# Optimization experiments

Hardware: AMD Instinct MI355X
Metric: run time of the kernel (lower is better)

## Reference

```python
import jax, jax.numpy as jnp
import numpy as np

NUM_REGIONS = 64
K_NEIGHBORS = 5
REGION_LAMBDA = 0.02
SPATIAL_LAMBDA = 0.0005


def setup_inputs() -> dict:
    key = jax.random.key(0)
    k1, k2, k3 = jax.random.split(key, 3)
    B = 16384
    c_points = jax.random.normal(k1, (B, 3), dtype=jnp.float32)
    coords_std = jax.random.normal(k2, (B, 3), dtype=jnp.float32)
    region_ids = jax.random.randint(k3, (B,), 0, NUM_REGIONS, dtype=jnp.int32)
    return {"c_points": c_points, "coords_std": coords_std, "region_ids": region_ids}


def _region_loss(c_points, region_ids):
    # Equivalent to per-region pairwise dispersion via segment reductions:
    # 2 * sum||c - mean_r||^2 / (max(n_r*(n_r-1)/2, 1) * xdim), summed over regions.
    dtype = c_points.dtype
    xdim = jnp.asarray(c_points.shape[1], dtype)
    ones = jnp.ones(c_points.shape[0], dtype)
    counts = jax.ops.segment_sum(ones, region_ids, num_segments=NUM_REGIONS)          # [R]
    sums = jax.ops.segment_sum(c_points, region_ids, num_segments=NUM_REGIONS)        # [R,3]
    sqs = jax.ops.segment_sum(c_points * c_points, region_ids, num_segments=NUM_REGIONS)  # [R,3]
    safe_n = jnp.maximum(counts, 1.0)
    mean = sums / safe_n[:, None]
    sum_sq_centered = jnp.sum(sqs - counts[:, None] * mean * mean, axis=1)             # [R]
    n_pairs = counts * (counts - 1.0) * 0.5
    denom = jnp.maximum(n_pairs, 1.0) * xdim
    per_region = jnp.where(counts > 1.0, 2.0 * sum_sq_centered / denom, 0.0)
    return jnp.asarray(REGION_LAMBDA, dtype) * jnp.sum(per_region)


def _spatial_loss(c_points, coords_std):
    # Dense pairwise squared distances, exclude self, KNN gather, mean squared diff of cuts.
    dtype = c_points.dtype
    B = coords_std.shape[0]
    xdim = jnp.asarray(c_points.shape[1], dtype)
    c2 = jnp.sum(coords_std * coords_std, axis=1, keepdims=True)                       # [B,1]
    d2 = c2 - 2.0 * (coords_std @ coords_std.T) + c2.T                                 # [B,B]
    big = jnp.max(d2) + 1.0
    diag = jnp.arange(B)
    d2 = d2.at[diag, diag].set(big)
    _, idxs = jax.lax.top_k(-d2, K_NEIGHBORS)                                          # [B,k]
    c_nb = c_points[idxs]                                                              # [B,k,3]
    diffs = c_points[:, None, :] - c_nb
    sq = jnp.sum(diffs * diffs, axis=2)                                                # [B,k]
    loss = jnp.mean(jnp.mean(sq, axis=1))
    return jnp.asarray(SPATIAL_LAMBDA, dtype) * (loss / jnp.maximum(xdim, 1.0))


def reference(c_points, coords_std, region_ids):
    return _region_loss(c_points, region_ids) + _spatial_loss(c_points, coords_std)
```

## Files before the change

kernel.cpp:

```cpp
#include <hip/hip_runtime.h>
#include <stdint.h>

#define B_N    16384
#define NREG   64
#define KNB    5
#define SAMPLE 4096
#define NSUB   16
#define SUBLEN (SAMPLE / NSUB)
#define NCH    32
#define CHLEN  (B_N / NCH)
#define MRGBLK 256
#define SENT   0xFFFF

static __device__ __forceinline__ float inf32() { return __int_as_float(0x7f800000); }
static __device__ __forceinline__ float med3(float a, float b, float c) {
    return __builtin_amdgcn_fmed3f(a, b, c);
}

#define MINS5(nv)                      \
    {                                  \
        s4 = med3(s3, s4, (nv));       \
        s3 = med3(s2, s3, (nv));       \
        s2 = med3(s1, s2, (nv));       \
        s1 = med3(s0, s1, (nv));       \
        s0 = fminf(s0, (nv));          \
    }

#define INS5(nv, jj)                                                        \
    {                                                                       \
        bool c4 = (nv) < s4, c3 = (nv) < s3, c2 = (nv) < s2,                \
             c1 = (nv) < s1, c0 = (nv) < s0;                                \
        s4 = c3 ? s3 : (c4 ? (nv) : s4);  i4 = c3 ? i3 : (c4 ? (jj) : i4);  \
        s3 = c2 ? s2 : (c3 ? (nv) : s3);  i3 = c2 ? i2 : (c3 ? (jj) : i3);  \
        s2 = c1 ? s1 : (c2 ? (nv) : s2);  i2 = c1 ? i1 : (c2 ? (jj) : i2);  \
        s1 = c0 ? s0 : (c1 ? (nv) : s1);  i1 = c0 ? i0 : (c1 ? (jj) : i1);  \
        s0 = c0 ? (nv) : s0;              i0 = c0 ? (jj) : i0;              \
    }

__global__ __launch_bounds__(256) void scan_region_kernel(const float* __restrict__ c,
                                                          const float* __restrict__ x,
                                                          const int* __restrict__ ids,
                                                          float4* __restrict__ pre,
                                                          float* __restrict__ tauv,
                                                          float* __restrict__ wsreg,
                                                          int* __restrict__ counter) {
    const int blk = blockIdx.x;
    const int tid = threadIdx.x;

    if (blk >= 1024) {
        const int r = blk - 1024;
        if (r == 0 && tid == 0) *counter = 0;
        {
            int j = r * 256 + tid;
            float jx = x[3 * j + 0], jy = x[3 * j + 1], jz = x[3 * j + 2];
            pre[j] = make_float4(-2.f * jx, -2.f * jy, -2.f * jz,
                                 jx * jx + jy * jy + jz * jz);
        }
        float cnt = 0.f, sx = 0.f, sy = 0.f, sz = 0.f, sxx = 0.f, syy = 0.f, szz = 0.f;
        for (int i = tid; i < B_N; i += 256) {
            int id = ids[i];
            float m = (id == r) ? 1.0f : 0.0f;
            float px = c[3 * i + 0], py = c[3 * i + 1], pz = c[3 * i + 2];
            cnt += m;
            sx += m * px;  sy += m * py;  sz += m * pz;
            sxx += m * px * px;  syy += m * py * py;  szz += m * pz * pz;
        }
        for (int off = 32; off > 0; off >>= 1) {
            cnt += __shfl_down(cnt, off);
            sx  += __shfl_down(sx, off);
            sy  += __shfl_down(sy, off);
            sz  += __shfl_down(sz, off);
            sxx += __shfl_down(sxx, off);
            syy += __shfl_down(syy, off);
            szz += __shfl_down(szz, off);
        }
        __shared__ float sb[4][7];
        const int lane = tid & 63, w = tid >> 6;
        if (lane == 0) {
            sb[w][0] = cnt; sb[w][1] = sx; sb[w][2] = sy; sb[w][3] = sz;
            sb[w][4] = sxx; sb[w][5] = syy; sb[w][6] = szz;
        }
        __syncthreads();
        if (tid == 0) {
            float C = 0, SX = 0, SY = 0, SZ = 0, SXX = 0, SYY = 0, SZZ = 0;
            for (int i = 0; i < 4; i++) {
                C += sb[i][0]; SX += sb[i][1]; SY += sb[i][2]; SZ += sb[i][3];
                SXX += sb[i][4]; SYY += sb[i][5]; SZZ += sb[i][6];
            }
            float safe = fmaxf(C, 1.0f);
            float mx = SX / safe, my = SY / safe, mz = SZ / safe;
            float ssc = (SXX - C * mx * mx) + (SYY - C * my * my) + (SZZ - C * mz * mz);
            float npairs = C * (C - 1.0f) * 0.5f;
            float denom = fmaxf(npairs, 1.0f) * 3.0f;
            wsreg[r] = (C > 1.0f) ? (2.0f * ssc / denom) : 0.0f;
        }
        return;
    }

    __shared__ float4 tile[SUBLEN];
    const int qb = blk & 63;
    const int sub = blk >> 6;
    const int q = qb * 256 + tid;
    const int j0 = sub * SUBLEN;
    {
        int j = j0 + tid;
        float jx = x[3 * j + 0], jy = x[3 * j + 1], jz = x[3 * j + 2];
        tile[tid] = make_float4(-2.f * jx, -2.f * jy, -2.f * jz,
                                jx * jx + jy * jy + jz * jz);
    }
    const float qx = x[3 * q + 0], qy = x[3 * q + 1], qz = x[3 * q + 2];
    __syncthreads();

    float s0 = inf32(), s1 = inf32(), s2 = inf32(), s3 = inf32(), s4 = inf32();

    for (int jb = 0; jb < SUBLEN; jb += 8) {
        float dt[8];
#pragma unroll
        for (int u = 0; u < 8; ++u) {
            float4 pj = tile[jb + u];
            dt[u] = fmaf(pj.x, qx, fmaf(pj.y, qy, fmaf(pj.z, qz, pj.w)));
        }
#pragma unroll
        for (int u = 0; u < 8; ++u) {
            float nv = ((j0 + jb + u) != q) ? dt[u] : inf32();
            MINS5(nv);
        }
    }
    tauv[(sub * 5 + 0) * B_N + q] = s0;
    tauv[(sub * 5 + 1) * B_N + q] = s1;
    tauv[(sub * 5 + 2) * B_N + q] = s2;
    tauv[(sub * 5 + 3) * B_N + q] = s3;
    tauv[(sub * 5 + 4) * B_N + q] = s4;
}

__global__ __launch_bounds__(256) void tau_merge_kernel(const float* __restrict__ tauv,
                                                        float* __restrict__ tau) {
    const int q = blockIdx.x * 256 + threadIdx.x;
    float s0 = inf32(), s1 = inf32(), s2 = inf32(), s3 = inf32(), s4 = inf32();
#pragma unroll 8
    for (int n = 0; n < NSUB * 5; ++n) {
        float v = tauv[n * B_N + q];
        MINS5(v);
    }
    int b = __float_as_int(s4);
    b += (b >= 0) ? 1 : -1;
    tau[q] = __int_as_float(b);
}

__global__ __launch_bounds__(256) void spatial_kernel(const float4* __restrict__ pre,
                                                      const float* __restrict__ tau,
                                                      unsigned short* __restrict__ cand) {
    __shared__ float4 tile[CHLEN];
    const int tid = threadIdx.x;
    const int qb = blockIdx.x & 63;
    const int ch = blockIdx.x >> 6;
    const int q = qb * 256 + tid;
    const int jbase = ch * CHLEN;

#pragma unroll
    for (int i = 0; i < CHLEN / 256; ++i)
        tile[tid + i * 256] = pre[jbase + tid + i * 256];

    const float4 pq = pre[q];
    const float qx = -0.5f * pq.x, qy = -0.5f * pq.y, qz = -0.5f * pq.z;
    const float t = tau[q];
    __syncthreads();

    float s0 = t, s1 = t, s2 = t, s3 = t, s4 = t;
    int i0 = SENT, i1 = SENT, i2 = SENT, i3 = SENT, i4 = SENT;

    for (int jb = 0; jb < CHLEN; jb += 8) {
        float dt[8];
#pragma unroll
        for (int u = 0; u < 8; ++u) {
            float4 pj = tile[jb + u];
            dt[u] = fmaf(pj.x, qx, fmaf(pj.y, qy, fmaf(pj.z, qz, pj.w)));
        }
        float m = fminf(fminf(fminf(dt[0], dt[1]), fminf(dt[2], dt[3])),
                        fminf(fminf(dt[4], dt[5]), fminf(dt[6], dt[7])));
        if (__builtin_expect(__any(m < s4), 0)) {
#pragma unroll
            for (int u = 0; u < 8; ++u) {
                if (__any(dt[u] < s4)) {
                    int j = jbase + jb + u;
                    bool p = (dt[u] < s4) && (j != q);
                    float nv = p ? dt[u] : inf32();
                    INS5(nv, j);
                }
            }
        }
    }
    cand[(ch * 5 + 0) * B_N + q] = (unsigned short)i0;
    cand[(ch * 5 + 1) * B_N + q] = (unsigned short)i1;
    cand[(ch * 5 + 2) * B_N + q] = (unsigned short)i2;
    cand[(ch * 5 + 3) * B_N + q] = (unsigned short)i3;
    cand[(ch * 5 + 4) * B_N + q] = (unsigned short)i4;
}

__global__ __launch_bounds__(256) void merge_kernel(const float* __restrict__ c,
                                                    const float4* __restrict__ pre,
                                                    const unsigned short* __restrict__ cand,
                                                    const float* __restrict__ wsreg,
                                                    float* __restrict__ spart,
                                                    int* __restrict__ counter,
                                                    float* __restrict__ out) {
    const int tid = threadIdx.x;
    const int blk = blockIdx.x;
    const int qloc = tid >> 2;
    const int part = tid & 3;
    const int q = blk * 64 + qloc;
    const float4 pq = pre[q];
    const float qx = -0.5f * pq.x, qy = -0.5f * pq.y, qz = -0.5f * pq.z;

    __shared__ float dm[64][4][5];
    __shared__ unsigned short im[64][4][5];

    {
        float s0 = inf32(), s1 = inf32(), s2 = inf32(), s3 = inf32(), s4 = inf32();
        int i0 = SENT & 0x3FFF, i1 = i0, i2 = i0, i3 = i0, i4 = i0;
        const int n0 = part * (NCH / 4) * 5;
#pragma unroll 8
        for (int n = n0; n < n0 + (NCH / 4) * 5; ++n) {
            int cd = (int)cand[n * B_N + q];
            int safe = cd & 0x3FFF;
            float4 pj = pre[safe];
            float d = fmaf(pj.x, qx, fmaf(pj.y, qy, fmaf(pj.z, qz, pj.w)));
            float nv = (cd != SENT) ? d : inf32();
            INS5(nv, safe);
        }
        dm[qloc][part][0] = s0; im[qloc][part][0] = (unsigned short)i0;
        dm[qloc][part][1] = s1; im[qloc][part][1] = (unsigned short)i1;
        dm[qloc][part][2] = s2; im[qloc][part][2] = (unsigned short)i2;
        dm[qloc][part][3] = s3; im[qloc][part][3] = (unsigned short)i3;
        dm[qloc][part][4] = s4; im[qloc][part][4] = (unsigned short)i4;
    }
    __syncthreads();

    float acc = 0.f;
    if (part == 0) {
        float s0 = inf32(), s1 = inf32(), s2 = inf32(), s3 = inf32(), s4 = inf32();
        int i0 = 0, i1 = 0, i2 = 0, i3 = 0, i4 = 0;
#pragma unroll
        for (int p = 0; p < 4; ++p)
#pragma unroll
            for (int k = 0; k < 5; ++k) {
                float nv = dm[qloc][p][k];
                int jj = (int)im[qloc][p][k];
                INS5(nv, jj);
            }
        const float cx = c[3 * q + 0], cy = c[3 * q + 1], cz = c[3 * q + 2];
        int ks[5] = {i0, i1, i2, i3, i4};
#pragma unroll
        for (int n = 0; n < KNB; ++n) {
            int nb = ks[n];
            float dx = cx - c[3 * nb + 0];
            float dy = cy - c[3 * nb + 1];
            float dz = cz - c[3 * nb + 2];
            acc += dx * dx + dy * dy + dz * dz;
        }
    }
    acc += __shfl_down(acc, 32);
    acc += __shfl_down(acc, 16);
    acc += __shfl_down(acc, 8);
    acc += __shfl_down(acc, 4);
    __shared__ float wsum[4];
    __shared__ int last;
    const int lane = tid & 63, w = tid >> 6;
    if (lane == 0) wsum[w] = acc;
    __syncthreads();
    if (tid == 0) {
        float bs = wsum[0] + wsum[1] + wsum[2] + wsum[3];
        atomicExch(&spart[blk], bs);
        __threadfence();
        int old = atomicAdd(counter, 1);
        last = (old == MRGBLK - 1);
    }
    __syncthreads();
    if (last) {
        float s = atomicAdd(&spart[tid], 0.0f);
        float r = (tid < NREG) ? wsreg[tid] : 0.f;
        for (int off = 32; off > 0; off >>= 1) {
            s += __shfl_down(s, off);
            r += __shfl_down(r, off);
        }
        __shared__ float fb[4];
        if (lane == 0) fb[w] = s;
        __syncthreads();
        if (tid == 0) {
            float S = fb[0] + fb[1] + fb[2] + fb[3];
            float spatial_mean = S / (float)(B_N * KNB);
            out[0] = 0.02f * r + 0.0005f * (spatial_mean / 3.0f);
        }
    }
}

extern "C" void kernel_launch(void* const* d_in, const int* in_sizes, int n_in,
                              void* d_out, int out_size, void* d_ws, size_t ws_size,
                              hipStream_t stream) {
    const float* c  = (const float*)d_in[0];
    const float* x  = (const float*)d_in[1];
    const int* ids  = (const int*)d_in[2];
    float* out = (float*)d_out;

    char* ws = (char*)d_ws;
    float4* pre = (float4*)ws;
    float* tauv = (float*)(ws + (size_t)B_N * 16);
    unsigned short* cand =
        (unsigned short*)((char*)tauv + (size_t)NSUB * 5 * B_N * 4);
    float* tau = (float*)((char*)cand + (size_t)NCH * 5 * B_N * 2);
    float* wsreg = tau + B_N;
    float* spart = wsreg + NREG;
    int* counter = (int*)(spart + MRGBLK);

    hipLaunchKernelGGL(scan_region_kernel, dim3(1088), dim3(256), 0, stream,
                       c, x, ids, pre, tauv, wsreg, counter);
    hipLaunchKernelGGL(tau_merge_kernel, dim3(64), dim3(256), 0, stream, tauv, tau);
    hipLaunchKernelGGL(spatial_kernel, dim3(64 * NCH), dim3(256), 0, stream, pre, tau, cand);
    hipLaunchKernelGGL(merge_kernel, dim3(MRGBLK), dim3(256), 0, stream, c, pre, cand,
                       wsreg, spart, counter, out);
}
```

Before: 92.45 us.

## Fuse tau merge, spatial scan and candidate merge into one kernel

The tau threshold merge is folded into the spatial kernel, so every block recomputes the per-query threshold from tauv instead of reading it from a separate kernel's output. The final candidate merge now runs in the last-arriving block of each query group, found through per-group atomic counters, and a global counter picks the block that does the final reduction. This removes two kernel launches and their inter-kernel gaps. In exchange, tauv reads are repeated 32 times over, and the final merge runs with one thread per query in only 64 blocks, which serializes the tail.

Result: slower. 139.6 us (+51.0%).

```diff
diff --git a/kernel.cpp b/kernel.cpp
--- a/kernel.cpp
+++ b/kernel.cpp
@@ -9,7 +9,6 @@
 #define SUBLEN (SAMPLE / NSUB)
 #define NCH    32
 #define CHLEN  (B_N / NCH)
-#define MRGBLK 256
 #define SENT   0xFFFF
 
 static __device__ __forceinline__ float inf32() { return __int_as_float(0x7f800000); }
@@ -43,13 +42,17 @@
                                                           float4* __restrict__ pre,
                                                           float* __restrict__ tauv,
                                                           float* __restrict__ wsreg,
+                                                          int* __restrict__ qbcount,
                                                           int* __restrict__ counter) {
     const int blk = blockIdx.x;
     const int tid = threadIdx.x;
 
     if (blk >= 1024) {
         const int r = blk - 1024;
-        if (r == 0 && tid == 0) *counter = 0;
+        if (tid == 0) {
+            qbcount[r] = 0;
+            if (r == 0) *counter = 0;
+        }
         {
             int j = r * 256 + tid;
             float jx = x[3 * j + 0], jy = x[3 * j + 1], jz = x[3 * j + 2];
@@ -133,23 +136,15 @@
     tauv[(sub * 5 + 4) * B_N + q] = s4;
 }
 
-__global__ __launch_bounds__(256) void tau_merge_kernel(const float* __restrict__ tauv,
-                                                        float* __restrict__ tau) {
-    const int q = blockIdx.x * 256 + threadIdx.x;
-    float s0 = inf32(), s1 = inf32(), s2 = inf32(), s3 = inf32(), s4 = inf32();
-#pragma unroll 8
-    for (int n = 0; n < NSUB * 5; ++n) {
-        float v = tauv[n * B_N + q];
-        MINS5(v);
-    }
-    int b = __float_as_int(s4);
-    b += (b >= 0) ? 1 : -1;
-    tau[q] = __int_as_float(b);
-}
-
-__global__ __launch_bounds__(256) void spatial_kernel(const float4* __restrict__ pre,
-                                                      const float* __restrict__ tau,
-                                                      unsigned short* __restrict__ cand) {
+__global__ __launch_bounds__(256) void spatial_merge_kernel(const float* __restrict__ c,
+                                                            const float4* __restrict__ pre,
+                                                            const float* __restrict__ tauv,
+                                                            unsigned short* __restrict__ cand,
+                                                            const float* __restrict__ wsreg,
+                                                            float* __restrict__ spart,
+                                                            int* __restrict__ qbcount,
+                                                            int* __restrict__ counter,
+                                                            float* __restrict__ out) {
     __shared__ float4 tile[CHLEN];
     const int tid = threadIdx.x;
     const int qb = blockIdx.x & 63;
@@ -163,64 +158,72 @@
 
     const float4 pq = pre[q];
     const float qx = -0.5f * pq.x, qy = -0.5f * pq.y, qz = -0.5f * pq.z;
-    const float t = tau[q];
-    __syncthreads();
-
-    float s0 = t, s1 = t, s2 = t, s3 = t, s4 = t;
-    int i0 = SENT, i1 = SENT, i2 = SENT, i3 = SENT, i4 = SENT;
-
-    for (int jb = 0; jb < CHLEN; jb += 8) {
-        float dt[8];
-#pragma unroll
-        for (int u = 0; u < 8; ++u) {
-            float4 pj = tile[jb + u];
-            dt[u] = fmaf(pj.x, qx, fmaf(pj.y, qy, fmaf(pj.z, qz, pj.w)));
-        }
-        float m = fminf(fminf(fminf(dt[0], dt[1]), fminf(dt[2], dt[3])),
-                        fminf(fminf(dt[4], dt[5]), fminf(dt[6], dt[7])));
-        if (__builtin_expect(__any(m < s4), 0)) {
+
+    float t;
+    {
+        float s0 = inf32(), s1 = inf32(), s2 = inf32(), s3 = inf32(), s4 = inf32();
+#pragma unroll 8
+        for (int n = 0; n < NSUB * 5; ++n) {
+            float v = tauv[n * B_N + q];
+            MINS5(v);
+        }
+        int b = __float_as_int(s4);
+        b += (b >= 0) ? 1 : -1;
+        t = __int_as_float(b);
+    }
+    __syncthreads();
+
+    {
+        float s0 = t, s1 = t, s2 = t, s3 = t, s4 = t;
+        int i0 = SENT, i1 = SENT, i2 = SENT, i3 = SENT, i4 = SENT;
+
+        for (int jb = 0; jb < CHLEN; jb += 8) {
+            float dt[8];
 #pragma unroll
             for (int u = 0; u < 8; ++u) {
-                if (__any(dt[u] < s4)) {
-                    int j = jbase + jb + u;
-                    bool p = (dt[u] < s4) && (j != q);
-                    float nv = p ? dt[u] : inf32();
-                    INS5(nv, j);
+                float4 pj = tile[jb + u];
+                dt[u] = fmaf(pj.x, qx, fmaf(pj.y, qy, fmaf(pj.z, qz, pj.w)));
+            }
+            float m = fminf(fminf(fminf(dt[0], dt[1]), fminf(dt[2], dt[3])),
+                            fminf(fminf(dt[4], dt[5]), fminf(dt[6], dt[7])));
+            if (__builtin_expect(__any(m < s4), 0)) {
+#pragma unroll
+                for (int u = 0; u < 8; ++u) {
+                    if (__any(dt[u] < s4)) {
+                        int j = jbase + jb + u;
+                        bool p = (dt[u] < s4) && (j != q);
+                        float nv = p ? dt[u] : inf32();
+                        INS5(nv, j);
+                    }
                 }
             }
         }
-    }
-    cand[(ch * 5 + 0) * B_N + q] = (unsigned short)i0;
-    cand[(ch * 5 + 1) * B_N + q] = (unsigned short)i1;
-    cand[(ch * 5 + 2) * B_N + q] = (unsigned short)i2;
-    cand[(ch * 5 + 3) * B_N + q] = (unsigned short)i3;
-    cand[(ch * 5 + 4) * B_N + q] = (unsigned short)i4;
-}
-
-__global__ __launch_bounds__(256) void merge_kernel(const float* __restrict__ c,
-                                                    const float4* __restrict__ pre,
-                                                    const unsigned short* __restrict__ cand,
-                                                    const float* __restrict__ wsreg,
-                                                    float* __restrict__ spart,
-                                                    int* __restrict__ counter,
-                                                    float* __restrict__ out) {
-    const int tid = threadIdx.x;
-    const int blk = blockIdx.x;
-    const int qloc = tid >> 2;
-    const int part = tid & 3;
-    const int q = blk * 64 + qloc;
-    const float4 pq = pre[q];
-    const float qx = -0.5f * pq.x, qy = -0.5f * pq.y, qz = -0.5f * pq.z;
-
-    __shared__ float dm[64][4][5];
-    __shared__ unsigned short im[64][4][5];
-
+        cand[(ch * 5 + 0) * B_N + q] = (unsigned short)i0;
+        cand[(ch * 5 + 1) * B_N + q] = (unsigned short)i1;
+        cand[(ch * 5 + 2) * B_N + q] = (unsigned short)i2;
+        cand[(ch * 5 + 3) * B_N + q] = (unsigned short)i3;
+        cand[(ch * 5 + 4) * B_N + q] = (unsigned short)i4;
+    }
+
+    __shared__ int lastqb;
+    __syncthreads();
+    if (tid == 0) {
+        __threadfence();
+        int old = atomicAdd(&qbcount[qb], 1);
+        lastqb = (old == NCH - 1);
+    }
+    __syncthreads();
+    if (!lastqb) return;
+
+    if (tid == 0) __threadfence();
+    __syncthreads();
+
+    float acc = 0.f;
     {
         float s0 = inf32(), s1 = inf32(), s2 = inf32(), s3 = inf32(), s4 = inf32();
-        int i0 = SENT & 0x3FFF, i1 = i0, i2 = i0, i3 = i0, i4 = i0;
-        const int n0 = part * (NCH / 4) * 5;
+        int i0 = 0, i1 = 0, i2 = 0, i3 = 0, i4 = 0;
 #pragma unroll 8
-        for (int n = n0; n < n0 + (NCH / 4) * 5; ++n) {
+        for (int n = 0; n < NCH * 5; ++n) {
             int cd = (int)cand[n * B_N + q];
             int safe = cd & 0x3FFF;
             float4 pj = pre[safe];
@@ -228,26 +231,6 @@
             float nv = (cd != SENT) ? d : inf32();
             INS5(nv, safe);
         }
-        dm[qloc][part][0] = s0; im[qloc][part][0] = (unsigned short)i0;
-        dm[qloc][part][1] = s1; im[qloc][part][1] = (unsigned short)i1;
-        dm[qloc][part][2] = s2; im[qloc][part][2] = (unsigned short)i2;
-        dm[qloc][part][3] = s3; im[qloc][part][3] = (unsigned short)i3;
-        dm[qloc][part][4] = s4; im[qloc][part][4] = (unsigned short)i4;
-    }
-    __syncthreads();
-
-    float acc = 0.f;
-    if (part == 0) {
-        float s0 = inf32(), s1 = inf32(), s2 = inf32(), s3 = inf32(), s4 = inf32();
-        int i0 = 0, i1 = 0, i2 = 0, i3 = 0, i4 = 0;
-#pragma unroll
-        for (int p = 0; p < 4; ++p)
-#pragma unroll
-            for (int k = 0; k < 5; ++k) {
-                float nv = dm[qloc][p][k];
-                int jj = (int)im[qloc][p][k];
-                INS5(nv, jj);
-            }
         const float cx = c[3 * q + 0], cy = c[3 * q + 1], cz = c[3 * q + 2];
         int ks[5] = {i0, i1, i2, i3, i4};
 #pragma unroll
@@ -259,37 +242,37 @@
             acc += dx * dx + dy * dy + dz * dz;
         }
     }
-    acc += __shfl_down(acc, 32);
-    acc += __shfl_down(acc, 16);
-    acc += __shfl_down(acc, 8);
-    acc += __shfl_down(acc, 4);
+    for (int off = 32; off > 0; off >>= 1) acc += __shfl_down(acc, off);
     __shared__ float wsum[4];
-    __shared__ int last;
+    __shared__ int lastall;
     const int lane = tid & 63, w = tid >> 6;
     if (lane == 0) wsum[w] = acc;
     __syncthreads();
     if (tid == 0) {
         float bs = wsum[0] + wsum[1] + wsum[2] + wsum[3];
-        atomicExch(&spart[blk], bs);
+        atomicExch(&spart[qb], bs);
         __threadfence();
         int old = atomicAdd(counter, 1);
-        last = (old == MRGBLK - 1);
-    }
-    __syncthreads();
-    if (last) {
-        float s = atomicAdd(&spart[tid], 0.0f);
+        lastall = (old == 63);
+    }
+    __syncthreads();
+    if (!lastall) return;
+
+    {
+        float s = (tid < 64) ? atomicAdd(&spart[tid], 0.0f) : 0.f;
         float r = (tid < NREG) ? wsreg[tid] : 0.f;
         for (int off = 32; off > 0; off >>= 1) {
             s += __shfl_down(s, off);
             r += __shfl_down(r, off);
         }
-        __shared__ float fb[4];
-        if (lane == 0) fb[w] = s;
+        __shared__ float fb[4][2];
+        if (lane == 0) { fb[w][0] = s; fb[w][1] = r; }
         __syncthreads();
         if (tid == 0) {
-            float S = fb[0] + fb[1] + fb[2] + fb[3];
+            float S = fb[0][0] + fb[1][0] + fb[2][0] + fb[3][0];
+            float R = fb[0][1] + fb[1][1] + fb[2][1] + fb[3][1];
             float spatial_mean = S / (float)(B_N * KNB);
-            out[0] = 0.02f * r + 0.0005f * (spatial_mean / 3.0f);
+            out[0] = 0.02f * R + 0.0005f * (spatial_mean / 3.0f);
         }
     }
 }
@@ -307,15 +290,13 @@
     float* tauv = (float*)(ws + (size_t)B_N * 16);
     unsigned short* cand =
         (unsigned short*)((char*)tauv + (size_t)NSUB * 5 * B_N * 4);
-    float* tau = (float*)((char*)cand + (size_t)NCH * 5 * B_N * 2);
-    float* wsreg = tau + B_N;
+    float* wsreg = (float*)((char*)cand + (size_t)NCH * 5 * B_N * 2);
     float* spart = wsreg + NREG;
-    int* counter = (int*)(spart + MRGBLK);
+    int* qbcount = (int*)(spart + 64);
+    int* counter = qbcount + 64;
 
     hipLaunchKernelGGL(scan_region_kernel, dim3(1088), dim3(256), 0, stream,
-                       c, x, ids, pre, tauv, wsreg, counter);
-    hipLaunchKernelGGL(tau_merge_kernel, dim3(64), dim3(256), 0, stream, tauv, tau);
-    hipLaunchKernelGGL(spatial_kernel, dim3(64 * NCH), dim3(256), 0, stream, pre, tau, cand);
-    hipLaunchKernelGGL(merge_kernel, dim3(MRGBLK), dim3(256), 0, stream, c, pre, cand,
-                       wsreg, spart, counter, out);
+                       c, x, ids, pre, tauv, wsreg, qbcount, counter);
+    hipLaunchKernelGGL(spatial_merge_kernel, dim3(64 * NCH), dim3(256), 0, stream,
+                       c, pre, tauv, cand, wsreg, spart, qbcount, counter, out);
 }
```

## Use packed FP32 FMA with paired SoA tiles for distance evaluation

Applied to the files above, without the earlier changes.

Reference points are stored in pairs (two x's, two y's, two z's, two norms) so that v_pk_fma_f32 computes two squared distances per instruction in both the sampling scan and the candidate spatial pass. The aim is to halve the FMA instruction count in these compute-bound loops. A second change drops the self-exclusion select in scan blocks whose tile cannot contain the query. Costs are an extra pre-pass writing the paired layout, inline asm, and more workspace.

New measurement: 103.4 us. +11.9%, slower.

```diff
diff --git a/kernel.cpp b/kernel.cpp
--- a/kernel.cpp
+++ b/kernel.cpp
@@ -12,9 +12,21 @@
 #define MRGBLK 256
 #define SENT   0xFFFF
 
+typedef __attribute__((ext_vector_type(2))) float f32x2;
+
 static __device__ __forceinline__ float inf32() { return __int_as_float(0x7f800000); }
 static __device__ __forceinline__ float med3(float a, float b, float c) {
     return __builtin_amdgcn_fmed3f(a, b, c);
+}
+static __device__ __forceinline__ f32x2 pk_fma(f32x2 a, f32x2 b, f32x2 c) {
+    f32x2 d;
+    asm("v_pk_fma_f32 %0, %1, %2, %3" : "=v"(d) : "v"(a), "v"(b), "v"(c));
+    return d;
+}
+static __device__ __forceinline__ f32x2 pdist(float4 A, float4 B,
+                                              f32x2 qx2, f32x2 qy2, f32x2 qz2) {
+    f32x2 X = {A.x, A.y}, Y = {A.z, A.w}, Z = {B.x, B.y}, W = {B.z, B.w};
+    return pk_fma(X, qx2, pk_fma(Y, qy2, pk_fma(Z, qz2, W)));
 }
 
 #define MINS5(nv)                      \
@@ -41,6 +53,8 @@
                                                           const float* __restrict__ x,
                                                           const int* __restrict__ ids,
                                                           float4* __restrict__ pre,
+                                                          float4* __restrict__ gA,
+                                                          float4* __restrict__ gB,
                                                           float* __restrict__ tauv,
                                                           float* __restrict__ wsreg,
                                                           int* __restrict__ counter) {
@@ -55,6 +69,14 @@
             float jx = x[3 * j + 0], jy = x[3 * j + 1], jz = x[3 * j + 2];
             pre[j] = make_float4(-2.f * jx, -2.f * jy, -2.f * jz,
                                  jx * jx + jy * jy + jz * jz);
+            if ((tid & 1) == 0) {
+                float kx = x[3 * j + 3], ky = x[3 * j + 4], kz = x[3 * j + 5];
+                int p = j >> 1;
+                gA[p] = make_float4(-2.f * jx, -2.f * kx, -2.f * jy, -2.f * ky);
+                gB[p] = make_float4(-2.f * jz, -2.f * kz,
+                                    jx * jx + jy * jy + jz * jz,
+                                    kx * kx + ky * ky + kz * kz);
+            }
         }
         float cnt = 0.f, sx = 0.f, sy = 0.f, sz = 0.f, sxx = 0.f, syy = 0.f, szz = 0.f;
         for (int i = tid; i < B_N; i += 256) {
@@ -97,33 +119,50 @@
         return;
     }
 
-    __shared__ float4 tile[SUBLEN];
+    __shared__ float4 tA[SUBLEN / 2], tB[SUBLEN / 2];
     const int qb = blk & 63;
     const int sub = blk >> 6;
     const int q = qb * 256 + tid;
     const int j0 = sub * SUBLEN;
-    {
+    if ((tid & 1) == 0) {
         int j = j0 + tid;
-        float jx = x[3 * j + 0], jy = x[3 * j + 1], jz = x[3 * j + 2];
-        tile[tid] = make_float4(-2.f * jx, -2.f * jy, -2.f * jz,
-                                jx * jx + jy * jy + jz * jz);
+        float ax = x[3 * j + 0], ay = x[3 * j + 1], az = x[3 * j + 2];
+        float bx = x[3 * j + 3], by = x[3 * j + 4], bz = x[3 * j + 5];
+        int p = tid >> 1;
+        tA[p] = make_float4(-2.f * ax, -2.f * bx, -2.f * ay, -2.f * by);
+        tB[p] = make_float4(-2.f * az, -2.f * bz,
+                            ax * ax + ay * ay + az * az,
+                            bx * bx + by * by + bz * bz);
     }
     const float qx = x[3 * q + 0], qy = x[3 * q + 1], qz = x[3 * q + 2];
+    const f32x2 qx2 = {qx, qx}, qy2 = {qy, qy}, qz2 = {qz, qz};
     __syncthreads();
 
     float s0 = inf32(), s1 = inf32(), s2 = inf32(), s3 = inf32(), s4 = inf32();
 
-    for (int jb = 0; jb < SUBLEN; jb += 8) {
-        float dt[8];
-#pragma unroll
-        for (int u = 0; u < 8; ++u) {
-            float4 pj = tile[jb + u];
-            dt[u] = fmaf(pj.x, qx, fmaf(pj.y, qy, fmaf(pj.z, qz, pj.w)));
-        }
-#pragma unroll
-        for (int u = 0; u < 8; ++u) {
-            float nv = ((j0 + jb + u) != q) ? dt[u] : inf32();
-            MINS5(nv);
+    if (sub != (qb & 15) || qb >= 16) {
+        for (int jb = 0; jb < SUBLEN; jb += 8) {
+            const int p0 = jb >> 1;
+            f32x2 d0 = pdist(tA[p0 + 0], tB[p0 + 0], qx2, qy2, qz2);
+            f32x2 d1 = pdist(tA[p0 + 1], tB[p0 + 1], qx2, qy2, qz2);
+            f32x2 d2 = pdist(tA[p0 + 2], tB[p0 + 2], qx2, qy2, qz2);
+            f32x2 d3 = pdist(tA[p0 + 3], tB[p0 + 3], qx2, qy2, qz2);
+            MINS5(d0.x); MINS5(d0.y); MINS5(d1.x); MINS5(d1.y);
+            MINS5(d2.x); MINS5(d2.y); MINS5(d3.x); MINS5(d3.y);
+        }
+    } else {
+        for (int jb = 0; jb < SUBLEN; jb += 8) {
+            const int p0 = jb >> 1;
+            f32x2 d0 = pdist(tA[p0 + 0], tB[p0 + 0], qx2, qy2, qz2);
+            f32x2 d1 = pdist(tA[p0 + 1], tB[p0 + 1], qx2, qy2, qz2);
+            f32x2 d2 = pdist(tA[p0 + 2], tB[p0 + 2], qx2, qy2, qz2);
+            f32x2 d3 = pdist(tA[p0 + 3], tB[p0 + 3], qx2, qy2, qz2);
+            float dv[8] = {d0.x, d0.y, d1.x, d1.y, d2.x, d2.y, d3.x, d3.y};
+#pragma unroll
+            for (int u = 0; u < 8; ++u) {
+                float nv = ((j0 + jb + u) != q) ? dv[u] : inf32();
+                MINS5(nv);
+            }
         }
     }
     tauv[(sub * 5 + 0) * B_N + q] = s0;
@@ -148,21 +187,23 @@
 }
 
 __global__ __launch_bounds__(256) void spatial_kernel(const float4* __restrict__ pre,
+                                                      const float4* __restrict__ gA,
+                                                      const float4* __restrict__ gB,
                                                       const float* __restrict__ tau,
                                                       unsigned short* __restrict__ cand) {
-    __shared__ float4 tile[CHLEN];
+    __shared__ float4 tA[CHLEN / 2], tB[CHLEN / 2];
     const int tid = threadIdx.x;
     const int qb = blockIdx.x & 63;
     const int ch = blockIdx.x >> 6;
     const int q = qb * 256 + tid;
     const int jbase = ch * CHLEN;
 
-#pragma unroll
-    for (int i = 0; i < CHLEN / 256; ++i)
-        tile[tid + i * 256] = pre[jbase + tid + i * 256];
+    tA[tid] = gA[(jbase >> 1) + tid];
+    tB[tid] = gB[(jbase >> 1) + tid];
 
     const float4 pq = pre[q];
     const float qx = -0.5f * pq.x, qy = -0.5f * pq.y, qz = -0.5f * pq.z;
+    const f32x2 qx2 = {qx, qx}, qy2 = {qy, qy}, qz2 = {qz, qz};
     const float t = tau[q];
     __syncthreads();
 
@@ -170,21 +211,21 @@
     int i0 = SENT, i1 = SENT, i2 = SENT, i3 = SENT, i4 = SENT;
 
     for (int jb = 0; jb < CHLEN; jb += 8) {
-        float dt[8];
-#pragma unroll
-        for (int u = 0; u < 8; ++u) {
-            float4 pj = tile[jb + u];
-            dt[u] = fmaf(pj.x, qx, fmaf(pj.y, qy, fmaf(pj.z, qz, pj.w)));
-        }
-        float m = fminf(fminf(fminf(dt[0], dt[1]), fminf(dt[2], dt[3])),
-                        fminf(fminf(dt[4], dt[5]), fminf(dt[6], dt[7])));
+        const int p0 = jb >> 1;
+        f32x2 d0 = pdist(tA[p0 + 0], tB[p0 + 0], qx2, qy2, qz2);
+        f32x2 d1 = pdist(tA[p0 + 1], tB[p0 + 1], qx2, qy2, qz2);
+        f32x2 d2 = pdist(tA[p0 + 2], tB[p0 + 2], qx2, qy2, qz2);
+        f32x2 d3 = pdist(tA[p0 + 3], tB[p0 + 3], qx2, qy2, qz2);
+        float m = fminf(fminf(fminf(d0.x, d0.y), fminf(d1.x, d1.y)),
+                        fminf(fminf(d2.x, d2.y), fminf(d3.x, d3.y)));
         if (__builtin_expect(__any(m < s4), 0)) {
+            float dv[8] = {d0.x, d0.y, d1.x, d1.y, d2.x, d2.y, d3.x, d3.y};
 #pragma unroll
             for (int u = 0; u < 8; ++u) {
-                if (__any(dt[u] < s4)) {
+                if (__any(dv[u] < s4)) {
                     int j = jbase + jb + u;
-                    bool p = (dt[u] < s4) && (j != q);
-                    float nv = p ? dt[u] : inf32();
+                    bool p = (dv[u] < s4) && (j != q);
+                    float nv = p ? dv[u] : inf32();
                     INS5(nv, j);
                 }
             }
@@ -304,7 +345,9 @@
 
     char* ws = (char*)d_ws;
     float4* pre = (float4*)ws;
-    float* tauv = (float*)(ws + (size_t)B_N * 16);
+    float4* gA  = (float4*)(ws + (size_t)B_N * 16);
+    float4* gB  = (float4*)(ws + (size_t)B_N * 24);
+    float* tauv = (float*)(ws + (size_t)B_N * 32);
     unsigned short* cand =
         (unsigned short*)((char*)tauv + (size_t)NSUB * 5 * B_N * 4);
     float* tau = (float*)((char*)cand + (size_t)NCH * 5 * B_N * 2);
@@ -313,9 +356,10 @@
     int* counter = (int*)(spart + MRGBLK);
 
     hipLaunchKernelGGL(scan_region_kernel, dim3(1088), dim3(256), 0, stream,
-                       c, x, ids, pre, tauv, wsreg, counter);
+                       c, x, ids, pre, gA, gB, tauv, wsreg, counter);
     hipLaunchKernelGGL(tau_merge_kernel, dim3(64), dim3(256), 0, stream, tauv, tau);
-    hipLaunchKernelGGL(spatial_kernel, dim3(64 * NCH), dim3(256), 0, stream, pre, tau, cand);
+    hipLaunchKernelGGL(spatial_kernel, dim3(64 * NCH), dim3(256), 0, stream,
+                       pre, gA, gB, tau, cand);
     hipLaunchKernelGGL(merge_kernel, dim3(MRGBLK), dim3(256), 0, stream, c, pre, cand,
                        wsreg, spart, counter, out);
 }
```

## Fuse tau merge into scan kernel via last-block atomic counter

Applied to the files above, without the earlier changes.

Removes the separate tau_merge kernel launch: each query block counts finished subchunks with an atomic, and the last one performs the 5-min merge and writes tau. It also moves the self-exclusion check out of the inner loop for subchunks that cannot contain the query. Counters are now zeroed with a memset before launch instead of inside the kernel, which adds a memset operation to the stream and a fence/atomic per block.

New measurement: 117.2 us. 1.27x slower.

```diff
diff --git a/kernel.cpp b/kernel.cpp
--- a/kernel.cpp
+++ b/kernel.cpp
@@ -42,14 +42,14 @@
                                                           const int* __restrict__ ids,
                                                           float4* __restrict__ pre,
                                                           float* __restrict__ tauv,
+                                                          float* __restrict__ tau,
                                                           float* __restrict__ wsreg,
-                                                          int* __restrict__ counter) {
+                                                          int* __restrict__ subcount) {
     const int blk = blockIdx.x;
     const int tid = threadIdx.x;
 
     if (blk >= 1024) {
         const int r = blk - 1024;
-        if (r == 0 && tid == 0) *counter = 0;
         {
             int j = r * 256 + tid;
             float jx = x[3 * j + 0], jy = x[3 * j + 1], jz = x[3 * j + 2];
@@ -111,40 +111,64 @@
     const float qx = x[3 * q + 0], qy = x[3 * q + 1], qz = x[3 * q + 2];
     __syncthreads();
 
-    float s0 = inf32(), s1 = inf32(), s2 = inf32(), s3 = inf32(), s4 = inf32();
-
-    for (int jb = 0; jb < SUBLEN; jb += 8) {
-        float dt[8];
-#pragma unroll
-        for (int u = 0; u < 8; ++u) {
-            float4 pj = tile[jb + u];
-            dt[u] = fmaf(pj.x, qx, fmaf(pj.y, qy, fmaf(pj.z, qz, pj.w)));
-        }
-#pragma unroll
-        for (int u = 0; u < 8; ++u) {
-            float nv = ((j0 + jb + u) != q) ? dt[u] : inf32();
-            MINS5(nv);
-        }
-    }
-    tauv[(sub * 5 + 0) * B_N + q] = s0;
-    tauv[(sub * 5 + 1) * B_N + q] = s1;
-    tauv[(sub * 5 + 2) * B_N + q] = s2;
-    tauv[(sub * 5 + 3) * B_N + q] = s3;
-    tauv[(sub * 5 + 4) * B_N + q] = s4;
-}
-
-__global__ __launch_bounds__(256) void tau_merge_kernel(const float* __restrict__ tauv,
-                                                        float* __restrict__ tau) {
-    const int q = blockIdx.x * 256 + threadIdx.x;
-    float s0 = inf32(), s1 = inf32(), s2 = inf32(), s3 = inf32(), s4 = inf32();
+    {
+        float s0 = inf32(), s1 = inf32(), s2 = inf32(), s3 = inf32(), s4 = inf32();
+        if (qb != sub) {
+            for (int jb = 0; jb < SUBLEN; jb += 8) {
+                float dt[8];
+#pragma unroll
+                for (int u = 0; u < 8; ++u) {
+                    float4 pj = tile[jb + u];
+                    dt[u] = fmaf(pj.x, qx, fmaf(pj.y, qy, fmaf(pj.z, qz, pj.w)));
+                }
+#pragma unroll
+                for (int u = 0; u < 8; ++u) MINS5(dt[u]);
+            }
+        } else {
+            for (int jb = 0; jb < SUBLEN; jb += 8) {
+                float dt[8];
+#pragma unroll
+                for (int u = 0; u < 8; ++u) {
+                    float4 pj = tile[jb + u];
+                    dt[u] = fmaf(pj.x, qx, fmaf(pj.y, qy, fmaf(pj.z, qz, pj.w)));
+                }
+#pragma unroll
+                for (int u = 0; u < 8; ++u) {
+                    float nv = ((j0 + jb + u) != q) ? dt[u] : inf32();
+                    MINS5(nv);
+                }
+            }
+        }
+        tauv[(sub * 5 + 0) * B_N + q] = s0;
+        tauv[(sub * 5 + 1) * B_N + q] = s1;
+        tauv[(sub * 5 + 2) * B_N + q] = s2;
+        tauv[(sub * 5 + 3) * B_N + q] = s3;
+        tauv[(sub * 5 + 4) * B_N + q] = s4;
+    }
+
+    __shared__ int lastsub;
+    __syncthreads();
+    if (tid == 0) {
+        __threadfence();
+        int old = atomicAdd(&subcount[qb], 1);
+        lastsub = (old == NSUB - 1);
+    }
+    __syncthreads();
+    if (!lastsub) return;
+    if (tid == 0) __threadfence();
+    __syncthreads();
+
+    {
+        float s0 = inf32(), s1 = inf32(), s2 = inf32(), s3 = inf32(), s4 = inf32();
 #pragma unroll 8
-    for (int n = 0; n < NSUB * 5; ++n) {
-        float v = tauv[n * B_N + q];
-        MINS5(v);
-    }
-    int b = __float_as_int(s4);
-    b += (b >= 0) ? 1 : -1;
-    tau[q] = __int_as_float(b);
+        for (int n = 0; n < NSUB * 5; ++n) {
+            float v = tauv[n * B_N + q];
+            MINS5(v);
+        }
+        int b = __float_as_int(s4);
+        b += (b >= 0) ? 1 : -1;
+        tau[q] = __int_as_float(b);
+    }
 }
 
 __global__ __launch_bounds__(256) void spatial_kernel(const float4* __restrict__ pre,
@@ -310,12 +334,15 @@
     float* tau = (float*)((char*)cand + (size_t)NCH * 5 * B_N * 2);
     float* wsreg = tau + B_N;
     float* spart = wsreg + NREG;
-    int* counter = (int*)(spart + MRGBLK);
+    int* subcount = (int*)(spart + MRGBLK);
+    int* counter = subcount + 64;
+
+    hipMemsetAsync(subcount, 0, 65 * sizeof(int), stream);
 
     hipLaunchKernelGGL(scan_region_kernel, dim3(1088), dim3(256), 0, stream,
-                       c, x, ids, pre, tauv, wsreg, counter);
-    hipLaunchKernelGGL(tau_merge_kernel, dim3(64), dim3(256), 0, stream, tauv, tau);
-    hipLaunchKernelGGL(spatial_kernel, dim3(64 * NCH), dim3(256), 0, stream, pre, tau, cand);
+                       c, x, ids, pre, tauv, tau, wsreg, subcount);
+    hipLaunchKernelGGL(spatial_kernel, dim3(64 * NCH), dim3(256), 0, stream,
+                       pre, tau, cand);
     hipLaunchKernelGGL(merge_kernel, dim3(MRGBLK), dim3(256), 0, stream, c, pre, cand,
                        wsreg, spart, counter, out);
 }
```
